# Performance work log

Hardware: AMD Instinct MI355X
Metric: run time of the kernel (lower is better)

The kernel has to match this reference:

```python
import jax, jax.numpy as jnp
import numpy as np

D = 384; NH = 4; FF = 1024; NL = 2
L_ENC = 750; T_AUD = 1500; VOCAB = 60; T_TXT = 256; B = 8; S_SPK = 8; GAMA = 1.0


def _conv1d(x, w, b, stride):
    y = jax.lax.conv_general_dilated(x, w, (stride,), [(1, 1)], dimension_numbers=("NCH", "OIH", "NCH"))
    return y + b[None, :, None]


def _ln(x, g, b):
    m = x.mean(-1, keepdims=True)
    v = ((x - m) ** 2).mean(-1, keepdims=True)
    return (x - m) * jax.lax.rsqrt(v + 1e-5) * g + b


def _enc_layer(x, qkv_w, qkv_b, ow, ob, f1w, f1b, f2w, f2b, g1, b1, g2, b2):
    Bq, L, d = x.shape
    hd = d // NH
    q, k, v = jnp.split(x @ qkv_w.T + qkv_b, 3, axis=-1)
    q = q.reshape(Bq, L, NH, hd); k = k.reshape(Bq, L, NH, hd); v = v.reshape(Bq, L, NH, hd)
    s = jnp.einsum("blhd,bmhd->bhlm", q, k) * np.float32(1.0 / np.sqrt(hd))
    a = jax.nn.softmax(s, axis=-1)
    ctx = jnp.einsum("bhlm,bmhd->blhd", a, v).reshape(Bq, L, d)
    x = _ln(x + ctx @ ow.T + ob, g1, b1)
    h = jax.nn.relu(x @ f1w.T + f1b) @ f2w.T + f2b
    return _ln(x + h, g2, b2)


def _gru(x, h, wih, whh, bih, bhh):
    gi = x @ wih.T + bih
    gh = h @ whh.T + bhh
    ir, iz, inn = jnp.split(gi, 3, axis=-1)
    hr, hz, hn = jnp.split(gh, 3, axis=-1)
    r = jax.nn.sigmoid(ir + hr)
    z = jax.nn.sigmoid(iz + hz)
    n = jnp.tanh(inn + r * hn)
    return (1.0 - z) * n + z * h


def _nll(logits, tgt):
    # torch F.nll_loss applied to raw scores (faithful to source), ignore_index=-100
    valid = (tgt != -100)
    idx = jnp.where(valid, tgt, 0)
    picked = jnp.take_along_axis(logits, idx[..., None], axis=-1)[..., 0]
    return -(picked * valid).sum() / jnp.maximum(valid.sum(), 1).astype(logits.dtype)


def _forward(fl, target_asr_ids, target_diar_ids, remat=False):
    (input_features, speaker_inventory, conv1_w, conv1_b, conv2_w, conv2_b,
     asr_qkv_w, asr_qkv_b, asr_attn_out_w, asr_attn_out_b, asr_ff1_w, asr_ff1_b,
     asr_ff2_w, asr_ff2_b, asr_ln1_g, asr_ln1_b, asr_ln2_g, asr_ln2_b,
     diar_qkv_w, diar_qkv_b, diar_attn_out_w, diar_attn_out_b, diar_ff1_w, diar_ff1_b,
     diar_ff2_w, diar_ff2_b, diar_ln1_g, diar_ln1_b, diar_ln2_g, diar_ln2_b,
     la_q_w, la_k_w, la_v_w, la_in_b, la_out_w, la_out_b, emb,
     asr_rnn_w_ih, asr_rnn_w_hh, asr_rnn_b_ih, asr_rnn_b_hh,
     diar_rnn_w_ih, diar_rnn_w_hh, diar_rnn_b_ih, diar_rnn_b_hh,
     asr_out_w, asr_out_b, d2a_w, d2a_b, h2a_w, h2a_b) = fl
    x = jax.nn.relu(_conv1d(input_features, conv1_w, conv1_b, 1))
    x = jax.nn.relu(_conv1d(x, conv2_w, conv2_b, 2))
    x = jnp.transpose(x, (0, 2, 1))  # [B, L_ENC, D]
    enc_asr = x
    for l in range(NL):
        enc_asr = _enc_layer(enc_asr, asr_qkv_w[l], asr_qkv_b[l], asr_attn_out_w[l], asr_attn_out_b[l],
                             asr_ff1_w[l], asr_ff1_b[l], asr_ff2_w[l], asr_ff2_b[l],
                             asr_ln1_g[l], asr_ln1_b[l], asr_ln2_g[l], asr_ln2_b[l])
    enc_diar = x
    for l in range(NL):
        enc_diar = _enc_layer(enc_diar, diar_qkv_w[l], diar_qkv_b[l], diar_attn_out_w[l], diar_attn_out_b[l],
                              diar_ff1_w[l], diar_ff1_b[l], diar_ff2_w[l], diar_ff2_b[l],
                              diar_ln1_g[l], diar_ln1_b[l], diar_ln2_g[l], diar_ln2_b[l])
    Bsz = x.shape[0]
    inv_norm = jnp.linalg.norm(speaker_inventory, axis=2)  # [B, S]

    def step(carry, tgt):
        token, asr_ctx, h_asr, h_diar, attns = carry
        e = emb[token]  # [B, D]
        h_asr = _gru(jnp.concatenate([asr_ctx, e], 1), h_asr,
                     asr_rnn_w_ih, asr_rnn_w_hh, asr_rnn_b_ih, asr_rnn_b_hh)
        # 1-dim MultiheadAttention: q=h_asr[:,:,None], k=prev attentions, v=enc_asr (vdim=384->1)
        q = h_asr[:, :, None] * la_q_w[0, 0] + la_in_b[0]   # [B, L, 1]
        k = attns * la_k_w[0, 0] + la_in_b[1]               # [B, L, 1]
        v = enc_asr @ la_v_w.T + la_in_b[2]                 # [B, L, 1]
        s = q @ jnp.swapaxes(k, 1, 2)                       # [B, L, L]; head_dim=1 -> scale 1
        a = jax.nn.softmax(s, axis=-1)
        attns_new = (a @ v) * la_out_w[0, 0] + la_out_b[0]  # [B, L, 1]
        w = attns_new[..., 0]
        asr_ctx_new = jnp.einsum("bld,bl->bd", enc_asr, w)
        spk_ctx = jnp.einsum("bld,bl->bd", enc_diar, w)
        h_diar_new = _gru(jnp.concatenate([spk_ctx, e], 1), h_diar,
                          diar_rnn_w_ih, diar_rnn_w_hh, diar_rnn_b_ih, diar_rnn_b_hh)
        sc = jnp.einsum("bsd,bd->bs", speaker_inventory, h_diar_new)
        hn = jnp.linalg.norm(h_diar_new, axis=1, keepdims=True)
        beta = jax.nn.softmax(sc / (hn * inv_norm), axis=1)
        spk_state = jnp.einsum("bsd,bs->bd", speaker_inventory, beta)
        logits = (asr_ctx_new + h_asr @ h2a_w.T + h2a_b + spk_state @ d2a_w.T + d2a_b) @ asr_out_w.T + asr_out_b
        next_tok = jnp.where(tgt == -100, 0, tgt)
        return (next_tok, asr_ctx_new, h_asr, h_diar_new, attns_new), (logits, beta)

    step_fn = jax.checkpoint(step) if remat else step
    init = (jnp.zeros((Bsz,), jnp.int32),
            jnp.zeros((Bsz, D), jnp.float32),
            jnp.zeros((Bsz, L_ENC), jnp.float32),
            jnp.zeros((Bsz, D), jnp.float32),
            jnp.zeros((Bsz, L_ENC, 1), jnp.float32))
    _, (logits_seq, beta_seq) = jax.lax.scan(step_fn, init, jnp.swapaxes(target_asr_ids, 0, 1))
    asr_outputs = jnp.swapaxes(logits_seq, 0, 1)   # [B, T, VOCAB]
    diar_outputs = jnp.swapaxes(beta_seq, 0, 1)    # [B, T, S]
    loss = _nll(asr_outputs, target_asr_ids) + GAMA * _nll(diar_outputs, target_diar_ids)
    return asr_outputs, diar_outputs, loss


def setup_inputs() -> dict:
    key = jax.random.key(0)
    cnt = [0]
    def p(shape, scale=0.05):
        cnt[0] += 1
        return jax.random.normal(jax.random.fold_in(key, cnt[0]), shape, dtype=jnp.float32) * scale
    inp = {}
    inp["input_features"] = p((B, 80, T_AUD), 1.0)
    inp["speaker_inventory"] = p((B, S_SPK, D), 1.0)
    inp["conv1_w"] = p((D, 80, 3)); inp["conv1_b"] = p((D,))
    inp["conv2_w"] = p((D, D, 3)); inp["conv2_b"] = p((D,))
    for pre in ("asr", "diar"):
        inp[pre + "_qkv_w"] = p((NL, 3 * D, D)); inp[pre + "_qkv_b"] = p((NL, 3 * D))
        inp[pre + "_attn_out_w"] = p((NL, D, D)); inp[pre + "_attn_out_b"] = p((NL, D))
        inp[pre + "_ff1_w"] = p((NL, FF, D)); inp[pre + "_ff1_b"] = p((NL, FF))
        inp[pre + "_ff2_w"] = p((NL, D, FF)); inp[pre + "_ff2_b"] = p((NL, D))
        inp[pre + "_ln1_g"] = jnp.ones((NL, D), jnp.float32); inp[pre + "_ln1_b"] = jnp.zeros((NL, D), jnp.float32)
        inp[pre + "_ln2_g"] = jnp.ones((NL, D), jnp.float32); inp[pre + "_ln2_b"] = jnp.zeros((NL, D), jnp.float32)
    inp["la_q_w"] = p((1, 1), 1.0); inp["la_k_w"] = p((1, 1), 1.0); inp["la_v_w"] = p((1, D))
    inp["la_in_b"] = p((3,)); inp["la_out_w"] = p((1, 1), 1.0); inp["la_out_b"] = p((1,))
    inp["emb"] = p((VOCAB, D), 1.0)
    inp["asr_rnn_w_ih"] = p((3 * L_ENC, 2 * D)); inp["asr_rnn_w_hh"] = p((3 * L_ENC, L_ENC))
    inp["asr_rnn_b_ih"] = p((3 * L_ENC,)); inp["asr_rnn_b_hh"] = p((3 * L_ENC,))
    inp["diar_rnn_w_ih"] = p((3 * D, 2 * D)); inp["diar_rnn_w_hh"] = p((3 * D, D))
    inp["diar_rnn_b_ih"] = p((3 * D,)); inp["diar_rnn_b_hh"] = p((3 * D,))
    inp["asr_out_w"] = p((VOCAB, D)); inp["asr_out_b"] = p((VOCAB,))
    inp["d2a_w"] = p((D, D)); inp["d2a_b"] = p((D,))
    inp["h2a_w"] = p((D, L_ENC)); inp["h2a_b"] = p((D,))
    inp["target_asr_ids"] = jax.random.randint(jax.random.fold_in(key, 9001), (B, T_TXT), 0, VOCAB, dtype=jnp.int32)
    inp["target_diar_ids"] = jax.random.randint(jax.random.fold_in(key, 9002), (B, T_TXT), 0, S_SPK, dtype=jnp.int32)
    return inp


def reference(input_features, speaker_inventory, conv1_w, conv1_b, conv2_w, conv2_b,
              asr_qkv_w, asr_qkv_b, asr_attn_out_w, asr_attn_out_b, asr_ff1_w, asr_ff1_b,
              asr_ff2_w, asr_ff2_b, asr_ln1_g, asr_ln1_b, asr_ln2_g, asr_ln2_b,
              diar_qkv_w, diar_qkv_b, diar_attn_out_w, diar_attn_out_b, diar_ff1_w, diar_ff1_b,
              diar_ff2_w, diar_ff2_b, diar_ln1_g, diar_ln1_b, diar_ln2_g, diar_ln2_b,
              la_q_w, la_k_w, la_v_w, la_in_b, la_out_w, la_out_b, emb,
              asr_rnn_w_ih, asr_rnn_w_hh, asr_rnn_b_ih, asr_rnn_b_hh,
              diar_rnn_w_ih, diar_rnn_w_hh, diar_rnn_b_ih, diar_rnn_b_hh,
              asr_out_w, asr_out_b, d2a_w, d2a_b, h2a_w, h2a_b,
              target_asr_ids, target_diar_ids):
    fl = (input_features, speaker_inventory, conv1_w, conv1_b, conv2_w, conv2_b,
          asr_qkv_w, asr_qkv_b, asr_attn_out_w, asr_attn_out_b, asr_ff1_w, asr_ff1_b,
          asr_ff2_w, asr_ff2_b, asr_ln1_g, asr_ln1_b, asr_ln2_g, asr_ln2_b,
          diar_qkv_w, diar_qkv_b, diar_attn_out_w, diar_attn_out_b, diar_ff1_w, diar_ff1_b,
          diar_ff2_w, diar_ff2_b, diar_ln1_g, diar_ln1_b, diar_ln2_g, diar_ln2_b,
          la_q_w, la_k_w, la_v_w, la_in_b, la_out_w, la_out_b, emb,
          asr_rnn_w_ih, asr_rnn_w_hh, asr_rnn_b_ih, asr_rnn_b_hh,
          diar_rnn_w_ih, diar_rnn_w_hh, diar_rnn_b_ih, diar_rnn_b_hh,
          asr_out_w, asr_out_b, d2a_w, d2a_b, h2a_w, h2a_b)
    return _forward(fl, target_asr_ids, target_diar_ids, remat=False)
```

## Files before the change

### kernel.cpp

```cpp
#include <hip/hip_runtime.h>
#include <math.h>

#define L_ENC 750
#define T_AUD 1500
#define DD    384
#define FF    1024
#define NHH   4
#define HDIM  96
#define VOCAB 60
#define T_TXT 256
#define BB    8
#define NB    480
#define TB    512

static __device__ __forceinline__ float sigmf(float x){ return 1.f/(1.f + __expf(-x)); }

static __device__ __forceinline__ float cld(const float* p){
  return __hip_atomic_load(p, __ATOMIC_RELAXED, __HIP_MEMORY_SCOPE_AGENT);
}
static __device__ __forceinline__ void cst(float* p, float v){
  __hip_atomic_store(p, v, __ATOMIC_RELAXED, __HIP_MEMORY_SCOPE_AGENT);
}

static __device__ __forceinline__ float bf2f(unsigned int v){
  union { unsigned int u; float f; } c; c.u = v << 16; return c.f;
}
static __device__ __forceinline__ unsigned short f2bf(float x){
  union { float f; unsigned int u; } c; c.f = x;
  unsigned int u = c.u + 0x7fffu + ((c.u >> 16) & 1u);
  return (unsigned short)(u >> 16);
}

static constexpr size_t O_X  = 0;
static constexpr size_t O_EA = 2304000;
static constexpr size_t O_ED = 4608000;
static constexpr size_t O_ST = 6912000;
static constexpr size_t oHASR = O_ST + 0;
static constexpr size_t oATT0 = O_ST + 6000;
static constexpr size_t oATT1 = O_ST + 12000;
static constexpr size_t oHD   = O_ST + 18000;
static constexpr size_t oACTX = O_ST + 21072;
static constexpr size_t oSCTX = O_ST + 27216;
static constexpr size_t oPREP = O_ST + 33360;
static constexpr size_t oGIA  = O_ST + 39504;
static constexpr size_t oGHA  = O_ST + 57504;
static constexpr size_t oGID  = O_ST + 75504;
static constexpr size_t oGHD  = O_ST + 84720;
static constexpr size_t oLACC = O_ST + 93936;
static constexpr size_t oVLA  = O_ST + 93944;
static constexpr size_t oINVN = O_ST + 99944;
static constexpr size_t oBAR  = O_ST + 100008;
static constexpr size_t oZ384 = O_ST + 104200;
static constexpr size_t O_SCR = O_ST + 105000;
static constexpr size_t oWIHAT_A = O_SCR + 0;
static constexpr size_t oWHHT_A  = O_SCR + 432000;
static constexpr size_t oWIHAT_D = O_SCR + 1278000;
static constexpr size_t oWHHT_D  = O_SCR + 1499184;
static constexpr size_t oH2ATh   = O_SCR + 1720368;
static constexpr size_t oAOT     = O_SCR + 1864368;
static constexpr size_t oEMBT    = O_SCR + 1887408;
static constexpr size_t oGEA     = O_SCR + 2673840;
static constexpr size_t oGED     = O_SCR + 7281840;
static constexpr size_t oDIB     = O_SCR + 9641136;
static constexpr size_t oEAh     = O_SCR + 9665712;
static constexpr size_t oEDh     = O_SCR + 10817712;
static constexpr size_t oTMPH    = O_SCR + 12000000;

__global__ void transpose_k(const float* __restrict__ in, int ldin, int R, int C,
                            float* __restrict__ out){
  __shared__ float t[32][33];
  int c0 = blockIdx.x*32, r0 = blockIdx.y*32;
  int x = threadIdx.x, y = threadIdx.y;
  for (int i = y; i < 32; i += 8){
    int r = r0 + i, c = c0 + x;
    t[i][x] = (r < R && c < C) ? in[(size_t)r*ldin + c] : 0.f;
  }
  __syncthreads();
  for (int i = y; i < 32; i += 8){
    int c = c0 + i, r = r0 + x;
    if (c < C && r < R) out[(size_t)c*R + r] = t[x][i];
  }
}

__global__ void packTbf_k(const float* __restrict__ in, int ldin, int R, int K,
                          unsigned short* __restrict__ out){
  __shared__ float tl[32][33];
  int k0 = blockIdx.x*32, r0 = blockIdx.y*32;
  int x = threadIdx.x, y = threadIdx.y;
  int K8 = ((K + 7) >> 3) << 3;
  for (int i = y; i < 32; i += 8){
    int r = r0 + i, k = k0 + x;
    tl[i][x] = (r < R && k < K) ? in[(size_t)r*ldin + k] : 0.f;
  }
  __syncthreads();
  for (int i = y; i < 32; i += 8){
    int k = k0 + i, r = r0 + x;
    if (k < K8 && r < R) out[((size_t)(k >> 3)*R + r)*8 + (k & 7)] = f2bf(tl[x][i]);
  }
}

__global__ __launch_bounds__(256) void cvtbf_k(const float* __restrict__ src,
    unsigned short* __restrict__ dst, int n4){
  int i = blockIdx.x*256 + threadIdx.x;
  if (i >= n4) return;
  float4 v = ((const float4*)src)[i];
  ushort4 o; o.x = f2bf(v.x); o.y = f2bf(v.y); o.z = f2bf(v.z); o.w = f2bf(v.w);
  ((ushort4*)dst)[i] = o;
}

__global__ void kt_k(const float* __restrict__ QKV, float* __restrict__ KT){
  __shared__ float t[32][33];
  int z = blockIdx.z; int b = z >> 2, h = z & 3;
  const float* in = QKV + (size_t)b*L_ENC*1152 + 384 + h*HDIM;
  float* out = KT + (size_t)z*HDIM*L_ENC;
  int c0 = blockIdx.x*32, r0 = blockIdx.y*32;
  int x = threadIdx.x, y = threadIdx.y;
  for (int i = y; i < 32; i += 8){
    int r = r0 + i, c = c0 + x;
    t[i][x] = (r < L_ENC && c < HDIM) ? in[(size_t)r*1152 + c] : 0.f;
  }
  __syncthreads();
  for (int i = y; i < 32; i += 8){
    int c = c0 + i, r = r0 + x;
    if (c < HDIM && r < L_ENC) out[(size_t)c*L_ENC + r] = t[x][i];
  }
}

template<int RELU, int HASRES>
__global__ __launch_bounds__(256) void gemm_k(
    const float* __restrict__ A, int lda, const float* __restrict__ W, int ldw,
    const float* __restrict__ bias, const float* __restrict__ Res,
    float* __restrict__ C, int ldc, int M, int N, int K)
{
  __shared__ __align__(16) float As[16][132];
  __shared__ __align__(16) float Ws[16][68];
  int tid = threadIdx.x;
  int row0 = blockIdx.y*128, col0 = blockIdx.x*64;
  int tx = tid & 15, ty = tid >> 4;
  int lr = tid >> 2, lk = (tid & 3)*4;
  float acc[8][4] = {};
  for (int k0 = 0; k0 < K; k0 += 16){
    float4 a0 = make_float4(0,0,0,0), a1 = make_float4(0,0,0,0), w0 = make_float4(0,0,0,0);
    int r0i = row0 + lr, r1i = row0 + 64 + lr, wri = col0 + lr;
    if (r0i < M) a0 = *(const float4*)(A + (size_t)r0i*lda + k0 + lk);
    if (r1i < M) a1 = *(const float4*)(A + (size_t)r1i*lda + k0 + lk);
    if (wri < N) w0 = *(const float4*)(W + (size_t)wri*ldw + k0 + lk);
    As[lk+0][lr] = a0.x; As[lk+1][lr] = a0.y; As[lk+2][lr] = a0.z; As[lk+3][lr] = a0.w;
    As[lk+0][64+lr] = a1.x; As[lk+1][64+lr] = a1.y; As[lk+2][64+lr] = a1.z; As[lk+3][64+lr] = a1.w;
    Ws[lk+0][lr] = w0.x; Ws[lk+1][lr] = w0.y; Ws[lk+2][lr] = w0.z; Ws[lk+3][lr] = w0.w;
    __syncthreads();
    #pragma unroll
    for (int k = 0; k < 16; k++){
      float4 b4 = *(const float4*)&Ws[k][tx*4];
      float4 a4 = *(const float4*)&As[k][ty*8];
      float4 a5 = *(const float4*)&As[k][ty*8+4];
      acc[0][0] += a4.x*b4.x; acc[0][1] += a4.x*b4.y; acc[0][2] += a4.x*b4.z; acc[0][3] += a4.x*b4.w;
      acc[1][0] += a4.y*b4.x; acc[1][1] += a4.y*b4.y; acc[1][2] += a4.y*b4.z; acc[1][3] += a4.y*b4.w;
      acc[2][0] += a4.z*b4.x; acc[2][1] += a4.z*b4.y; acc[2][2] += a4.z*b4.z; acc[2][3] += a4.z*b4.w;
      acc[3][0] += a4.w*b4.x; acc[3][1] += a4.w*b4.y; acc[3][2] += a4.w*b4.z; acc[3][3] += a4.w*b4.w;
      acc[4][0] += a5.x*b4.x; acc[4][1] += a5.x*b4.y; acc[4][2] += a5.x*b4.z; acc[4][3] += a5.x*b4.w;
      acc[5][0] += a5.y*b4.x; acc[5][1] += a5.y*b4.y; acc[5][2] += a5.y*b4.z; acc[5][3] += a5.y*b4.w;
      acc[6][0] += a5.z*b4.x; acc[6][1] += a5.z*b4.y; acc[6][2] += a5.z*b4.z; acc[6][3] += a5.z*b4.w;
      acc[7][0] += a5.w*b4.x; acc[7][1] += a5.w*b4.y; acc[7][2] += a5.w*b4.z; acc[7][3] += a5.w*b4.w;
    }
    __syncthreads();
  }
  #pragma unroll
  for (int ii = 0; ii < 8; ii++){
    int m = row0 + ty*8 + ii;
    if (m >= M) continue;
    #pragma unroll
    for (int jj = 0; jj < 4; jj++){
      int n = col0 + tx*4 + jj;
      if (n >= N) continue;
      float v = acc[ii][jj] + bias[n];
      if (HASRES) v += Res[(size_t)m*ldc + n];
      if (RELU) v = fmaxf(v, 0.f);
      C[(size_t)m*ldc + n] = v;
    }
  }
}

__global__ void im2col1(const float* __restrict__ in, float* __restrict__ P){
  int t = blockIdx.x, b = blockIdx.y, i = threadIdx.x;
  if (i >= 240) return;
  int ic = i/3, kt = i - ic*3;
  int p = t + kt - 1;
  P[((size_t)(b*T_AUD + t))*240 + i] = (p >= 0 && p < T_AUD) ? in[((size_t)(b*80 + ic))*T_AUD + p] : 0.f;
}

__global__ __launch_bounds__(384) void im2col2(const float* __restrict__ X1T, float* __restrict__ P){
  int t = blockIdx.x, b = blockIdx.y, ic = threadIdx.x;
  size_t ob = ((size_t)(b*L_ENC + t))*1152 + (size_t)ic*3;
  #pragma unroll
  for (int kt = 0; kt < 3; kt++){
    int p = 2*t + kt - 1;
    P[ob + kt] = (p >= 0 && p < T_AUD) ? X1T[((size_t)(b*T_AUD + p))*DD + ic] : 0.f;
  }
}

__global__ __launch_bounds__(256) void dup_k(const float* __restrict__ src,
    float* __restrict__ a, float* __restrict__ b){
  size_t i = (size_t)blockIdx.x*256 + threadIdx.x;
  float4 v = ((const float4*)src)[i];
  ((float4*)a)[i] = v;
  ((float4*)b)[i] = v;
}

__global__ __launch_bounds__(128) void ln_k(float* __restrict__ X, const float* __restrict__ g,
                                            const float* __restrict__ bt){
  int r = blockIdx.x, tid = threadIdx.x;
  float* p = X + (size_t)r*DD;
  float v0 = p[tid], v1 = p[tid+128], v2 = p[tid+256];
  __shared__ float red[128];
  red[tid] = v0+v1+v2; __syncthreads();
  for (int k = 64; k > 0; k >>= 1){ if (tid < k) red[tid] += red[tid+k]; __syncthreads(); }
  float m = red[0] * (1.f/384.f);
  __syncthreads();
  float d0 = v0-m, d1 = v1-m, d2 = v2-m;
  red[tid] = d0*d0 + d1*d1 + d2*d2; __syncthreads();
  for (int k = 64; k > 0; k >>= 1){ if (tid < k) red[tid] += red[tid+k]; __syncthreads(); }
  float rs = rsqrtf(red[0]*(1.f/384.f) + 1e-5f);
  p[tid]     = d0*rs*g[tid]     + bt[tid];
  p[tid+128] = d1*rs*g[tid+128] + bt[tid+128];
  p[tid+256] = d2*rs*g[tid+256] + bt[tid+256];
}

__global__ __launch_bounds__(1024) void attn_enc(const float* __restrict__ QKV,
    const float* __restrict__ KT, float* __restrict__ ctx){
  int b = blockIdx.z, h = blockIdx.y, i0 = blockIdx.x*16;
  int tid = threadIdx.x, lane = tid & 63, wv = tid >> 6;
  __shared__ float q_s[16][96];
  __shared__ float p_s[16][752];
  __shared__ float den_s[16];
  for (int idx = tid; idx < 16*96; idx += 1024){
    int r2 = idx/96, c = idx - r2*96; int i = i0 + r2;
    q_s[r2][c] = (i < L_ENC) ? QKV[((size_t)(b*L_ENC + i))*1152 + h*HDIM + c]*0.10206207f : 0.f;
  }
  __syncthreads();
  int i = i0 + wv;
  const float* ktb = KT + ((size_t)(b*4 + h))*HDIM*L_ENC;
  if (i < L_ENC){
    float sr[12] = {0,0,0,0,0,0,0,0,0,0,0,0};
    for (int c = 0; c < 96; c++){
      float qc = q_s[wv][c];
      const float* kr = ktb + c*L_ENC + lane;
      #pragma unroll
      for (int jt = 0; jt < 12; jt++) sr[jt] += qc*kr[jt*64];
    }
    float mx = -1e30f;
    #pragma unroll
    for (int jt = 0; jt < 12; jt++){ if (lane + jt*64 < L_ENC) mx = fmaxf(mx, sr[jt]); }
    #pragma unroll
    for (int o = 32; o > 0; o >>= 1) mx = fmaxf(mx, __shfl_xor(mx, o));
    float den = 0.f;
    #pragma unroll
    for (int jt = 0; jt < 12; jt++){
      int j = lane + jt*64;
      if (j < L_ENC){ float e = __expf(sr[jt]-mx); p_s[wv][j] = e; den += e; }
    }
    #pragma unroll
    for (int o = 32; o > 0; o >>= 1) den += __shfl_xor(den, o);
    if (lane == 0) den_s[wv] = den;
  }
  __syncthreads();
  if (i < L_ENC){
    float idn = 1.f/den_s[wv];
    const float* vb = QKV + (size_t)b*L_ENC*1152 + 768 + h*HDIM;
    float a0 = 0.f, a1 = 0.f;
    for (int j = 0; j < L_ENC; j++){
      float pj = p_s[wv][j];
      const float* vr = vb + (size_t)j*1152;
      a0 += pj*vr[lane];
      if (lane < 32) a1 += pj*vr[lane + 64];
    }
    size_t ob = ((size_t)(b*L_ENC + i))*DD + h*HDIM;
    ctx[ob + lane] = a0*idn;
    if (lane < 32) ctx[ob + lane + 64] = a1*idn;
  }
}

__global__ __launch_bounds__(384) void embed_k(const float* __restrict__ emb,
    const int* __restrict__ tgtA, float* __restrict__ E){
  int row = blockIdx.x; int t = row >> 3, b = row & 7;
  int tok = 0;
  if (t > 0){ int v = tgtA[b*T_TXT + t - 1]; tok = (v == -100) ? 0 : v; }
  E[(size_t)row*DD + threadIdx.x] = emb[(size_t)tok*DD + threadIdx.x];
}

__global__ __launch_bounds__(256) void vla_k(const float* __restrict__ EA,
    const float* __restrict__ lav, const float* __restrict__ lain, float* __restrict__ VLA){
  int row = blockIdx.x*4 + (threadIdx.x >> 6);
  int lane = threadIdx.x & 63;
  if (row >= BB*L_ENC) return;
  const float* p = EA + (size_t)row*DD;
  float s = 0.f;
  for (int d = lane; d < DD; d += 64) s += p[d]*lav[d];
  #pragma unroll
  for (int o = 32; o > 0; o >>= 1) s += __shfl_xor(s, o);
  if (lane == 0) VLA[row] = s + lain[2];
}

__global__ void invn_k(const float* __restrict__ inv, float* __restrict__ INVN){
  int row = blockIdx.x; int lane = threadIdx.x;
  float s = 0.f;
  for (int d = lane; d < DD; d += 64){ float v = inv[(size_t)row*DD + d]; s += v*v; }
  #pragma unroll
  for (int o = 32; o > 0; o >>= 1) s += __shfl_xor(s, o);
  if (lane == 0) INVN[row] = sqrtf(s);
}

struct DecParams {
  float* ws; float* out;
  const float* ABHH; const float* DBHH;
  const float* SPK;  const float* AOB;
  const float* LAQ; const float* LAK; const float* LAIB; const float* LAOW; const float* LAOB;
  const float* H2AB; const float* D2AB;
  const int* TGTA; const int* TGTD;
};

static __device__ __forceinline__ void gbar(unsigned* s, unsigned epoch){
  __syncthreads();
  int tid = threadIdx.x;
  if (blockIdx.x == 0){
    if (tid > 0 && tid < NB){
      while (__hip_atomic_load(&s[tid*4], __ATOMIC_RELAXED, __HIP_MEMORY_SCOPE_AGENT) < epoch)
        __builtin_amdgcn_s_sleep(4);
    }
    __syncthreads();
    if (tid < NB)
      __hip_atomic_store(&s[(512 + tid)*4], epoch, __ATOMIC_RELAXED, __HIP_MEMORY_SCOPE_AGENT);
  } else {
    if (tid == 0){
      __hip_atomic_store(&s[blockIdx.x*4], epoch, __ATOMIC_RELAXED, __HIP_MEMORY_SCOPE_AGENT);
      while (__hip_atomic_load(&s[(512 + blockIdx.x)*4], __ATOMIC_RELAXED, __HIP_MEMORY_SCOPE_AGENT) < epoch)
        __builtin_amdgcn_s_sleep(4);
    }
    __syncthreads();
  }
}

#define FMA8(acc, s_, base) { const float4 b0_ = *(const float4*)&(base)[0]; const float4 b1_ = *(const float4*)&(base)[4]; \
  acc[0]+=b0_.x*(s_); acc[1]+=b0_.y*(s_); acc[2]+=b0_.z*(s_); acc[3]+=b0_.w*(s_); \
  acc[4]+=b1_.x*(s_); acc[5]+=b1_.y*(s_); acc[6]+=b1_.z*(s_); acc[7]+=b1_.w*(s_); }

#define GFMA8(acc, wv_, a_) { \
  FMA8(acc, bf2f(wv_.x & 0xffffu), (a_)+0);  FMA8(acc, bf2f(wv_.x >> 16), (a_)+8); \
  FMA8(acc, bf2f(wv_.y & 0xffffu), (a_)+16); FMA8(acc, bf2f(wv_.y >> 16), (a_)+24); \
  FMA8(acc, bf2f(wv_.z & 0xffffu), (a_)+32); FMA8(acc, bf2f(wv_.z >> 16), (a_)+40); \
  FMA8(acc, bf2f(wv_.w & 0xffffu), (a_)+48); FMA8(acc, bf2f(wv_.w >> 16), (a_)+56); }

#define ACC8(acc, ev_, s_) { \
  acc[0]+=bf2f(ev_.x&0xffffu)*(s_); acc[1]+=bf2f(ev_.x>>16)*(s_); \
  acc[2]+=bf2f(ev_.y&0xffffu)*(s_); acc[3]+=bf2f(ev_.y>>16)*(s_); \
  acc[4]+=bf2f(ev_.z&0xffffu)*(s_); acc[5]+=bf2f(ev_.z>>16)*(s_); \
  acc[6]+=bf2f(ev_.w&0xffffu)*(s_); acc[7]+=bf2f(ev_.w>>16)*(s_); }

template<int NR, int KH, int KOH>
__device__ void gates_fn(int task, const unsigned short* __restrict__ WIT,
                         const unsigned short* __restrict__ WHT,
                         const float* __restrict__ ctxv, const float* __restrict__ hv,
                         const float* __restrict__ GE, const float* __restrict__ bhh,
                         float* __restrict__ GI, float* __restrict__ GH, int t, float* SM)
{
  float* ac  = SM;
  float* hh  = SM + 3072;
  float* pgi = SM + 3072 + KOH*64;
  float* pgh = pgi + 4096;
  int tid = threadIdx.x;
  for (int idx = tid; idx < 3072; idx += TB){ int b = idx/384, k = idx - b*384; ac[k*8+b] = cld(&ctxv[idx]); }
  for (int idx = tid; idx < KH*8;  idx += TB){ int b = idx/KH,  k = idx - b*KH;  hh[k*8+b] = cld(&hv[idx]); }
  for (int idx = KH*8 + tid; idx < KOH*64; idx += TB) hh[idx] = 0.f;
  __syncthreads();
  int rl = tid & 15, kp = tid >> 4;
  int r = task*16 + rl;
  float gi[8] = {}, gh[8] = {};
  if (r < NR){
    const uint4* W4 = (const uint4*)WIT;
    int q0 = (kp*48) >> 5, q1 = ((kp+1)*48) >> 5;
    for (int q = q0; q < q1; q++){
      uint4 wq = W4[(size_t)q*NR + r];
      const float* a = &ac[q*64];
      GFMA8(gi, wq, a);
    }
    const uint4* WH4 = (const uint4*)WHT;
    int h0 = (kp*KOH) >> 5, h1 = ((kp+1)*KOH) >> 5;
    for (int q = h0; q < h1; q++){
      uint4 wq = WH4[(size_t)q*NR + r];
      const float* a = &hh[q*64];
      GFMA8(gh, wq, a);
    }
  }
  #pragma unroll
  for (int b = 0; b < 8; b++){ pgi[(kp*16+rl)*8 + b] = gi[b]; pgh[(kp*16+rl)*8 + b] = gh[b]; }
  __syncthreads();
  if (tid < 128){
    int rl2 = tid & 15, bb = tid >> 4;
    int rr = task*16 + rl2;
    if (rr < NR){
      float s1 = 0.f, s2 = 0.f;
      #pragma unroll
      for (int kq = 0; kq < 32; kq++){ s1 += pgi[(kq*16+rl2)*8+bb]; s2 += pgh[(kq*16+rl2)*8+bb]; }
      cst(&GI[(size_t)bb*NR + rr], s1 + GE[((size_t)t*8 + bb)*NR + rr]);
      cst(&GH[(size_t)bb*NR + rr], s2 + bhh[rr]);
    }
  }
  __syncthreads();
}

__device__ void phase_hattn_ctx(int bid, int t, float* ws,
                                const unsigned short* __restrict__ EAh,
                                const unsigned short* __restrict__ EDh,
                                const unsigned short* __restrict__ H2h,
                                const DecParams& P, float* SM)
{
  float* kk = SM;
  float* vv = SM + 768;
  float* wl = SM + 1536;
  float* hl = SM + 1552;
  float* part = SM + 1568;
  int tid = threadIdx.x;
  int b = bid & 7, chunk = bid >> 3;
  int i0 = chunk*13; int n = L_ENC - i0; if (n > 13) n = 13;
  const float* acur = ws + ((t & 1) ? oATT1 : oATT0);
  float*       anxt = ws + ((t & 1) ? oATT0 : oATT1);
  const float* GIAp = ws + oGIA; const float* GHAp = ws + oGHA;
  float* HASRp = ws + oHASR;
  const float* VLAp = ws + oVLA;
  float kw = P.LAK[0], kb = P.LAIB[1];
  for (int j = tid; j < L_ENC; j += TB){
    kk[j] = cld(&acur[b*L_ENC + j])*kw + kb;
    vv[j] = VLAp[b*L_ENC + j];
  }
  __syncthreads();
  int wv = tid >> 6, lane = tid & 63;
  float laq = P.LAQ[0], li0 = P.LAIB[0], low = P.LAOW[0], lob = P.LAOB[0];
  for (int il = wv; il < n; il += 8){
    int i = i0 + il;
    int base = b*2250 + i;
    float rr = sigmf(cld(&GIAp[base]) + cld(&GHAp[base]));
    float zz = sigmf(cld(&GIAp[base+750]) + cld(&GHAp[base+750]));
    float nn = tanhf(cld(&GIAp[base+1500]) + rr*cld(&GHAp[base+1500]));
    float h = (1.f - zz)*nn + zz*cld(&HASRp[b*L_ENC + i]);
    float q = h*laq + li0;
    float sr[12]; float mx = -1e30f;
    #pragma unroll
    for (int jt = 0; jt < 12; jt++){
      int j = lane + jt*64;
      float s = (j < L_ENC) ? q*kk[j] : -1e30f;
      sr[jt] = s; mx = fmaxf(mx, s);
    }
    #pragma unroll
    for (int o = 32; o > 0; o >>= 1) mx = fmaxf(mx, __shfl_xor(mx, o));
    float se = 0.f, sv = 0.f;
    #pragma unroll
    for (int jt = 0; jt < 12; jt++){
      int j = lane + jt*64;
      if (j < L_ENC){ float e = __expf(sr[jt] - mx); se += e; sv += e*vv[j]; }
    }
    #pragma unroll
    for (int o = 32; o > 0; o >>= 1){ se += __shfl_xor(se, o); sv += __shfl_xor(sv, o); }
    if (lane == 0){
      cst(&HASRp[b*L_ENC + i], h);
      float w = (sv/se)*low + lob;
      cst(&anxt[b*L_ENC + i], w);
      wl[il] = w; hl[il] = h;
    }
  }
  __syncthreads();
  if (tid < 480){
    int lg = tid / 48, oct = tid - lg*48;
    int d0 = oct*8;
    float a8[8] = {}, s8[8] = {}, h8[8] = {};
    for (int j = lg; j < n; j += 10){
      size_t ro = ((size_t)(b*L_ENC + i0 + j))*DD + d0;
      float wj = wl[j], hj = hl[j];
      uint4 e1 = *(const uint4*)&EAh[ro];
      ACC8(a8, e1, wj);
      uint4 e2 = *(const uint4*)&EDh[ro];
      ACC8(s8, e2, wj);
      uint4 e3 = *(const uint4*)&H2h[(size_t)(i0 + j)*DD + d0];
      ACC8(h8, e3, hj);
    }
    float* pp = part + (size_t)(lg*48 + oct)*24;
    #pragma unroll
    for (int e = 0; e < 8; e++){ pp[e] = a8[e]; pp[8+e] = s8[e]; pp[16+e] = h8[e]; }
  }
  __syncthreads();
  if (tid < 96){
    int oct = tid >> 1, e = (tid & 1)*4;
    float ra[4] = {}, rs[4] = {}, rh[4] = {};
    #pragma unroll
    for (int lg = 0; lg < 10; lg++){
      const float* pp = part + (size_t)(lg*48 + oct)*24;
      #pragma unroll
      for (int jj = 0; jj < 4; jj++){
        ra[jj] += pp[e+jj]; rs[jj] += pp[8+e+jj]; rh[jj] += pp[16+e+jj];
      }
    }
    int par = t & 1;
    int d0 = tid*4;
    float* A = &ws[oACTX + par*3072 + b*DD + d0];
    float* S = &ws[oSCTX + par*3072 + b*DD + d0];
    float* Pr = &ws[oPREP + par*3072 + b*DD + d0];
    atomicAdd(&A[0], ra[0]); atomicAdd(&A[1], ra[1]); atomicAdd(&A[2], ra[2]); atomicAdd(&A[3], ra[3]);
    atomicAdd(&S[0], rs[0]); atomicAdd(&S[1], rs[1]); atomicAdd(&S[2], rs[2]); atomicAdd(&S[3], rs[3]);
    atomicAdd(&Pr[0], ra[0]+rh[0]); atomicAdd(&Pr[1], ra[1]+rh[1]);
    atomicAdd(&Pr[2], ra[2]+rh[2]); atomicAdd(&Pr[3], ra[3]+rh[3]);
  }
  __syncthreads();
}

__device__ void phase_final(int b, int t, float* ws, const float* prep,
                            const DecParams& P, float* SM)
{
  float* hd_s = SM;
  float* pre_s = SM + 384;
  float* red = SM + 768;
  float* beta_s = SM + 1280;
  float* sc_s = SM + 1288;
  float* part2 = SM + 1296;
  int tid = threadIdx.x;
  bool act = tid < DD;
  const float* GIDp = ws + oGID; const float* GHDp = ws + oGHD;
  float* HDp = ws + oHD;
  float h = 0.f;
  if (act){
    int base = b*1152 + tid;
    float rr = sigmf(cld(&GIDp[base]) + cld(&GHDp[base]));
    float zz = sigmf(cld(&GIDp[base+384]) + cld(&GHDp[base+384]));
    float nn = tanhf(cld(&GIDp[base+768]) + rr*cld(&GHDp[base+768]));
    h = (1.f - zz)*nn + zz*cld(&HDp[b*DD + tid]);
    hd_s[tid] = h; cst(&HDp[b*DD + tid], h);
  }
  red[tid] = act ? h*h : 0.f;
  __syncthreads();
  for (int s = 256; s > 0; s >>= 1){ if (tid < s) red[tid] += red[tid+s]; __syncthreads(); }
  float hn = sqrtf(red[0]);
  int sg = tid >> 6, lane = tid & 63;
  float ps = 0.f;
  for (int j = lane; j < DD; j += 64) ps += P.SPK[((size_t)(b*8 + sg))*DD + j]*hd_s[j];
  #pragma unroll
  for (int o = 32; o > 0; o >>= 1) ps += __shfl_xor(ps, o);
  if (lane == 0) sc_s[sg] = ps / (hn * ws[oINVN + b*8 + sg]);
  __syncthreads();
  if (tid == 0){
    float mx = -1e30f;
    for (int s2 = 0; s2 < 8; s2++) mx = fmaxf(mx, sc_s[s2]);
    float sm = 0.f;
    for (int s2 = 0; s2 < 8; s2++){ float e = __expf(sc_s[s2] - mx); beta_s[s2] = e; sm += e; }
    float isv = 1.f/sm;
    for (int s2 = 0; s2 < 8; s2++) beta_s[s2] *= isv;
    int td = P.TGTD[b*T_TXT + t];
    if (td != -100){ atomicAdd(&ws[oLACC+2], beta_s[td]); atomicAdd(&ws[oLACC+3], 1.f); }
  }
  __syncthreads();
  if (tid < 8) P.out[122880 + ((size_t)(b*T_TXT + t))*8 + tid] = beta_s[tid];
  if (act){
    float p = cld(&prep[b*DD + tid]);
    const float* Mb = ws + oDIB + (size_t)(b*8)*DD + tid;
    #pragma unroll
    for (int s2 = 0; s2 < 8; s2++) p += beta_s[s2]*Mb[(size_t)s2*DD];
    pre_s[tid] = p;
  }
  __syncthreads();
  {
    int vg = tid >> 6, v = tid & 63;
    float pl = 0.f;
    if (v < VOCAB){
      const float* AOTp = ws + oAOT;
      int d0 = vg*48;
      for (int d2 = d0; d2 < d0+48; d2++) pl += pre_s[d2]*AOTp[d2*VOCAB + v];
    }
    part2[vg*64 + v] = pl;
  }
  __syncthreads();
  if (tid < VOCAB){
    float lg = P.AOB[tid];
    #pragma unroll
    for (int g = 0; g < 8; g++) lg += part2[g*64 + tid];
    P.out[((size_t)(b*T_TXT + t))*VOCAB + tid] = lg;
    int ta = P.TGTA[b*T_TXT + t];
    if (ta == tid) atomicAdd(&ws[oLACC+0], lg);
    if (tid == 0 && ta != -100) atomicAdd(&ws[oLACC+1], 1.f);
  }
  __syncthreads();
}

__global__ __launch_bounds__(TB, 4) void dec_loop(DecParams P)
{
  __shared__ __align__(16) float SM[17280];
  int bid = blockIdx.x;
  float* ws = P.ws;
  unsigned* slots = (unsigned*)(ws + oBAR);
  unsigned ep = 0;
  const unsigned short* WIA = (const unsigned short*)(ws + oWIHAT_A);
  const unsigned short* WHA = (const unsigned short*)(ws + oWHHT_A);
  const unsigned short* WID = (const unsigned short*)(ws + oWIHAT_D);
  const unsigned short* WHD = (const unsigned short*)(ws + oWHHT_D);
  const unsigned short* EAh = (const unsigned short*)(ws + oEAh);
  const unsigned short* EDh = (const unsigned short*)(ws + oEDh);
  const unsigned short* H2h = (const unsigned short*)(ws + oH2ATh);

  if (bid < 141)
    gates_fn<2250,750,94>(bid, WIA, WHA, ws+oACTX, ws+oHASR,
                          ws+oGEA, P.ABHH, ws+oGIA, ws+oGHA, 0, SM);
  else if (bid < 149){
    int b = bid - 141;
    for (int d = threadIdx.x; d < DD; d += TB)
      cst(&ws[oPREP + b*DD + d], P.H2AB[d] + P.D2AB[d]);
  }
  gbar(slots, ++ep);

  for (int t = 0; t <= T_TXT; t++){
    if (t < T_TXT && bid < 464) phase_hattn_ctx(bid, t, ws, EAh, EDh, H2h, P, SM);
    else if (bid >= 464 && bid < 472 && t >= 1)
      phase_final(bid - 464, t - 1, ws, ws + oPREP + ((t-1) & 1)*3072, P, SM);
    gbar(slots, ++ep);
    if (t == T_TXT) break;

    if (bid < 72)
      gates_fn<1152,384,48>(bid, WID, WHD, ws+oSCTX+(t&1)*3072, ws+oHD,
                            ws+oGED, P.DBHH, ws+oGID, ws+oGHD, t, SM);
    else if (bid < 213){
      if (t + 1 < T_TXT)
        gates_fn<2250,750,94>(bid-72, WIA, WHA, ws+oACTX+(t&1)*3072, ws+oHASR,
                              ws+oGEA, P.ABHH, ws+oGIA, ws+oGHA, t+1, SM);
    } else if (bid < 221 && t + 1 < T_TXT){
      int b = bid - 213, par = (t + 1) & 1;
      for (int d = threadIdx.x; d < DD; d += TB){
        cst(&ws[oACTX + par*3072 + b*DD + d], 0.f);
        cst(&ws[oSCTX + par*3072 + b*DD + d], 0.f);
        cst(&ws[oPREP + par*3072 + b*DD + d], P.H2AB[d] + P.D2AB[d]);
      }
    }
    gbar(slots, ++ep);
  }
}

__global__ void loss_final_k(const float* __restrict__ lacc, float* __restrict__ out){
  if (threadIdx.x == 0 && blockIdx.x == 0){
    float la = lacc[0]/fmaxf(lacc[1], 1.f);
    float ld = lacc[2]/fmaxf(lacc[3], 1.f);
    out[139264] = -(la + ld);
  }
}

extern "C" void kernel_launch(void* const* d_in, const int* in_sizes, int n_in,
                              void* d_out, int out_size, void* d_ws, size_t ws_size,
                              hipStream_t stream)
{
  (void)in_sizes; (void)n_in; (void)out_size; (void)ws_size;
  float* ws  = (float*)d_ws;
  float* out = (float*)d_out;

  const float* IN0   = (const float*)d_in[0];
  const float* SPK   = (const float*)d_in[1];
  const float* C1W   = (const float*)d_in[2];
  const float* C1B   = (const float*)d_in[3];
  const float* C2W   = (const float*)d_in[4];
  const float* C2B   = (const float*)d_in[5];
  const float* LAQ   = (const float*)d_in[30];
  const float* LAK   = (const float*)d_in[31];
  const float* LAV   = (const float*)d_in[32];
  const float* LAIB  = (const float*)d_in[33];
  const float* LAOW  = (const float*)d_in[34];
  const float* LAOB  = (const float*)d_in[35];
  const float* EMB   = (const float*)d_in[36];
  const float* AWIH  = (const float*)d_in[37];
  const float* AWHH  = (const float*)d_in[38];
  const float* ABIH  = (const float*)d_in[39];
  const float* ABHH  = (const float*)d_in[40];
  const float* DWIH  = (const float*)d_in[41];
  const float* DWHH  = (const float*)d_in[42];
  const float* DBIH  = (const float*)d_in[43];
  const float* DBHH  = (const float*)d_in[44];
  const float* AOW   = (const float*)d_in[45];
  const float* AOB   = (const float*)d_in[46];
  const float* D2AW  = (const float*)d_in[47];
  const float* D2AB  = (const float*)d_in[48];
  const float* H2AW  = (const float*)d_in[49];
  const float* H2AB  = (const float*)d_in[50];
  const int*   TGTA  = (const int*)d_in[51];
  const int*   TGTD  = (const int*)d_in[52];

  const size_t S_QKV = O_SCR;
  const size_t S_KT  = O_SCR + 6912000;
  const size_t S_CTX = O_SCR + 9216000;
  const size_t S_Y   = O_SCR + 11520000;
  const size_t S_H   = O_SCR + 13824000;
  const size_t X1T   = S_KT;
  const size_t Pc1   = S_H;
  const size_t Pc2   = S_QKV;

  hipMemsetAsync((void*)(ws + O_ST), 0, 105000*sizeof(float), stream);

  im2col1<<<dim3(1500,8), 256, 0, stream>>>(IN0, ws + Pc1);
  gemm_k<1,0><<<dim3(6,94), 256, 0, stream>>>(ws+Pc1, 240, C1W, 240, C1B, nullptr, ws+X1T, 384, 12000, 384, 240);
  im2col2<<<dim3(750,8), 384, 0, stream>>>(ws+X1T, ws+Pc2);
  gemm_k<1,0><<<dim3(6,47), 256, 0, stream>>>(ws+Pc2, 1152, C2W, 1152, C2B, nullptr, ws+O_X, 384, 6000, 384, 1152);

  dup_k<<<2250, 256, 0, stream>>>(ws+O_X, ws+O_EA, ws+O_ED);

  auto enc_layer = [&](float* Xb, const float* qw, const float* qb, const float* ow,
                       const float* ob, const float* f1w, const float* f1b,
                       const float* f2w, const float* f2b,
                       const float* g1, const float* b1, const float* g2, const float* b2){
    gemm_k<0,0><<<dim3(18,47), 256, 0, stream>>>(Xb, 384, qw, 384, qb, nullptr, ws+S_QKV, 1152, 6000, 1152, 384);
    kt_k<<<dim3(3,24,32), dim3(32,8), 0, stream>>>(ws+S_QKV, ws+S_KT);
    attn_enc<<<dim3(47,4,8), 1024, 0, stream>>>(ws+S_QKV, ws+S_KT, ws+S_CTX);
    gemm_k<0,1><<<dim3(6,47), 256, 0, stream>>>(ws+S_CTX, 384, ow, 384, ob, Xb, ws+S_Y, 384, 6000, 384, 384);
    ln_k<<<6000, 128, 0, stream>>>(ws+S_Y, g1, b1);
    gemm_k<1,0><<<dim3(16,47), 256, 0, stream>>>(ws+S_Y, 384, f1w, 384, f1b, nullptr, ws+S_H, 1024, 6000, 1024, 384);
    gemm_k<0,1><<<dim3(6,47), 256, 0, stream>>>(ws+S_H, 1024, f2w, 1024, f2b, ws+S_Y, Xb, 384, 6000, 384, 1024);
    ln_k<<<6000, 128, 0, stream>>>(Xb, g2, b2);
  };
  for (int st = 0; st < 2; st++){
    int base = (st == 0) ? 6 : 18;
    float* Xb = ws + ((st == 0) ? O_EA : O_ED);
    const float* qkvw = (const float*)d_in[base+0];
    const float* qkvb = (const float*)d_in[base+1];
    const float* aow  = (const float*)d_in[base+2];
    const float* aob2 = (const float*)d_in[base+3];
    const float* f1w  = (const float*)d_in[base+4];
    const float* f1b  = (const float*)d_in[base+5];
    const float* f2w  = (const float*)d_in[base+6];
    const float* f2b  = (const float*)d_in[base+7];
    const float* g1   = (const float*)d_in[base+8];
    const float* b1   = (const float*)d_in[base+9];
    const float* g2   = (const float*)d_in[base+10];
    const float* b2   = (const float*)d_in[base+11];
    for (int l = 0; l < 2; l++){
      enc_layer(Xb, qkvw + (size_t)l*1152*384, qkvb + (size_t)l*1152,
                aow + (size_t)l*384*384, aob2 + (size_t)l*384,
                f1w + (size_t)l*1024*384, f1b + (size_t)l*1024,
                f2w + (size_t)l*384*1024, f2b + (size_t)l*384,
                g1 + (size_t)l*384, b1 + (size_t)l*384, g2 + (size_t)l*384, b2 + (size_t)l*384);
    }
  }

  packTbf_k<<<dim3(12,71), dim3(32,8), 0, stream>>>(AWIH, 768, 2250, 384, (unsigned short*)(ws+oWIHAT_A));
  packTbf_k<<<dim3(24,71), dim3(32,8), 0, stream>>>(AWHH, 750, 2250, 750, (unsigned short*)(ws+oWHHT_A));
  packTbf_k<<<dim3(12,36), dim3(32,8), 0, stream>>>(DWIH, 768, 1152, 384, (unsigned short*)(ws+oWIHAT_D));
  packTbf_k<<<dim3(12,36), dim3(32,8), 0, stream>>>(DWHH, 384, 1152, 384, (unsigned short*)(ws+oWHHT_D));
  transpose_k<<<dim3(24,12), dim3(32,8), 0, stream>>>(H2AW, 750, 384, 750, ws+oTMPH);
  cvtbf_k<<<282, 256, 0, stream>>>(ws+oTMPH, (unsigned short*)(ws+oH2ATh), 72000);
  transpose_k<<<dim3(12,2),  dim3(32,8), 0, stream>>>(AOW, 384, 60, 384, ws+oAOT);
  embed_k<<<2048, 384, 0, stream>>>(EMB, TGTA, ws+oEMBT);
  gemm_k<0,0><<<dim3(36,16), 256, 0, stream>>>(ws+oEMBT, 384, AWIH+384, 768, ABIH, nullptr, ws+oGEA, 2250, 2048, 2250, 384);
  gemm_k<0,0><<<dim3(18,16), 256, 0, stream>>>(ws+oEMBT, 384, DWIH+384, 768, DBIH, nullptr, ws+oGED, 1152, 2048, 1152, 384);
  gemm_k<0,0><<<dim3(6,1), 256, 0, stream>>>(SPK, 384, D2AW, 384, ws+oZ384, nullptr, ws+oDIB, 384, 64, 384, 384);
  vla_k<<<1500, 256, 0, stream>>>(ws+O_EA, LAV, LAIB, ws+oVLA);
  invn_k<<<64, 64, 0, stream>>>(SPK, ws+oINVN);
  cvtbf_k<<<2250, 256, 0, stream>>>(ws+O_EA, (unsigned short*)(ws+oEAh), 576000);
  cvtbf_k<<<2250, 256, 0, stream>>>(ws+O_ED, (unsigned short*)(ws+oEDh), 576000);

  DecParams DP;
  DP.ws = ws; DP.out = out;
  DP.ABHH = ABHH; DP.DBHH = DBHH; DP.SPK = SPK; DP.AOB = AOB;
  DP.LAQ = LAQ; DP.LAK = LAK; DP.LAIB = LAIB; DP.LAOW = LAOW; DP.LAOB = LAOB;
  DP.H2AB = H2AB; DP.D2AB = D2AB; DP.TGTA = TGTA; DP.TGTD = TGTD;
  dec_loop<<<dim3(NB), dim3(TB), 0, stream>>>(DP);

  loss_final_k<<<1, 64, 0, stream>>>(ws+oLACC, out);
}
```

Baseline: 21.25 ms.

## Split attention and context reduction into separate phases without atomics

```diff
diff --git a/kernel.cpp b/kernel.cpp
--- a/kernel.cpp
+++ b/kernel.cpp
@@ -350,12 +350,6 @@
   FMA8(acc, bf2f(wv_.z & 0xffffu), (a_)+32); FMA8(acc, bf2f(wv_.z >> 16), (a_)+40); \
   FMA8(acc, bf2f(wv_.w & 0xffffu), (a_)+48); FMA8(acc, bf2f(wv_.w >> 16), (a_)+56); }
 
-#define ACC8(acc, ev_, s_) { \
-  acc[0]+=bf2f(ev_.x&0xffffu)*(s_); acc[1]+=bf2f(ev_.x>>16)*(s_); \
-  acc[2]+=bf2f(ev_.y&0xffffu)*(s_); acc[3]+=bf2f(ev_.y>>16)*(s_); \
-  acc[4]+=bf2f(ev_.z&0xffffu)*(s_); acc[5]+=bf2f(ev_.z>>16)*(s_); \
-  acc[6]+=bf2f(ev_.w&0xffffu)*(s_); acc[7]+=bf2f(ev_.w>>16)*(s_); }
-
 template<int NR, int KH, int KOH>
 __device__ void gates_fn(int task, const unsigned short* __restrict__ WIT,
                          const unsigned short* __restrict__ WHT,
@@ -408,17 +402,10 @@
   __syncthreads();
 }
 
-__device__ void phase_hattn_ctx(int bid, int t, float* ws,
-                                const unsigned short* __restrict__ EAh,
-                                const unsigned short* __restrict__ EDh,
-                                const unsigned short* __restrict__ H2h,
-                                const DecParams& P, float* SM)
+__device__ void phase_hattn(int bid, int t, float* ws, const DecParams& P, float* SM)
 {
   float* kk = SM;
   float* vv = SM + 768;
-  float* wl = SM + 1536;
-  float* hl = SM + 1552;
-  float* part = SM + 1568;
   int tid = threadIdx.x;
   int b = bid & 7, chunk = bid >> 3;
   int i0 = chunk*13; int n = L_ENC - i0; if (n > 13) n = 13;
@@ -462,51 +449,58 @@
     for (int o = 32; o > 0; o >>= 1){ se += __shfl_xor(se, o); sv += __shfl_xor(sv, o); }
     if (lane == 0){
       cst(&HASRp[b*L_ENC + i], h);
-      float w = (sv/se)*low + lob;
-      cst(&anxt[b*L_ENC + i], w);
-      wl[il] = w; hl[il] = h;
-    }
-  }
-  __syncthreads();
-  if (tid < 480){
-    int lg = tid / 48, oct = tid - lg*48;
-    int d0 = oct*8;
-    float a8[8] = {}, s8[8] = {}, h8[8] = {};
-    for (int j = lg; j < n; j += 10){
-      size_t ro = ((size_t)(b*L_ENC + i0 + j))*DD + d0;
-      float wj = wl[j], hj = hl[j];
-      uint4 e1 = *(const uint4*)&EAh[ro];
-      ACC8(a8, e1, wj);
-      uint4 e2 = *(const uint4*)&EDh[ro];
-      ACC8(s8, e2, wj);
-      uint4 e3 = *(const uint4*)&H2h[(size_t)(i0 + j)*DD + d0];
-      ACC8(h8, e3, hj);
-    }
-    float* pp = part + (size_t)(lg*48 + oct)*24;
-    #pragma unroll
-    for (int e = 0; e < 8; e++){ pp[e] = a8[e]; pp[8+e] = s8[e]; pp[16+e] = h8[e]; }
-  }
-  __syncthreads();
-  if (tid < 96){
-    int oct = tid >> 1, e = (tid & 1)*4;
-    float ra[4] = {}, rs[4] = {}, rh[4] = {};
-    #pragma unroll
-    for (int lg = 0; lg < 10; lg++){
-      const float* pp = part + (size_t)(lg*48 + oct)*24;
-      #pragma unroll
-      for (int jj = 0; jj < 4; jj++){
-        ra[jj] += pp[e+jj]; rs[jj] += pp[8+e+jj]; rh[jj] += pp[16+e+jj];
-      }
-    }
-    int par = t & 1;
-    int d0 = tid*4;
-    float* A = &ws[oACTX + par*3072 + b*DD + d0];
-    float* S = &ws[oSCTX + par*3072 + b*DD + d0];
-    float* Pr = &ws[oPREP + par*3072 + b*DD + d0];
-    atomicAdd(&A[0], ra[0]); atomicAdd(&A[1], ra[1]); atomicAdd(&A[2], ra[2]); atomicAdd(&A[3], ra[3]);
-    atomicAdd(&S[0], rs[0]); atomicAdd(&S[1], rs[1]); atomicAdd(&S[2], rs[2]); atomicAdd(&S[3], rs[3]);
-    atomicAdd(&Pr[0], ra[0]+rh[0]); atomicAdd(&Pr[1], ra[1]+rh[1]);
-    atomicAdd(&Pr[2], ra[2]+rh[2]); atomicAdd(&Pr[3], ra[3]+rh[3]);
+      cst(&anxt[b*L_ENC + i], (sv/se)*low + lob);
+    }
+  }
+  __syncthreads();
+}
+
+__device__ void phase_ctx(int bid, int t, float* ws,
+                          const unsigned short* __restrict__ EAh,
+                          const unsigned short* __restrict__ EDh,
+                          const unsigned short* __restrict__ H2h,
+                          const DecParams& P, float* SM)
+{
+  float* wl   = SM;
+  float* hl   = SM + 768;
+  float* reda = SM + 1536;
+  float* reds = SM + 2048;
+  float* redh = SM + 2560;
+  int tid = threadIdx.x;
+  int b = bid & 7, dc = bid >> 3;
+  int d0 = dc*32;
+  const float* anxt = ws + ((t & 1) ? oATT0 : oATT1);
+  const float* HASRp = ws + oHASR;
+  for (int j = tid; j < L_ENC; j += TB){
+    wl[j] = cld(&anxt[b*L_ENC + j]);
+    hl[j] = cld(&HASRp[b*L_ENC + j]);
+  }
+  __syncthreads();
+  int ls = tid >> 5, dx = tid & 31;
+  int d = d0 + dx;
+  const unsigned short* EAb = EAh + (size_t)b*L_ENC*DD + d;
+  const unsigned short* EDb = EDh + (size_t)b*L_ENC*DD + d;
+  const unsigned short* H2b = H2h + d;
+  float a = 0.f, s = 0.f, hp = 0.f;
+  for (int l = ls; l < L_ENC; l += 16){
+    size_t lo = (size_t)l*DD;
+    float wj = wl[l], hj = hl[l];
+    a  += bf2f(EAb[lo])*wj;
+    s  += bf2f(EDb[lo])*wj;
+    hp += bf2f(H2b[lo])*hj;
+  }
+  reda[tid] = a; reds[tid] = s; redh[tid] = hp;
+  __syncthreads();
+  if (tid < 32){
+    float ra = 0.f, rs = 0.f, rh = 0.f;
+    #pragma unroll
+    for (int q = 0; q < 16; q++){
+      ra += reda[q*32+tid]; rs += reds[q*32+tid]; rh += redh[q*32+tid];
+    }
+    int dd = d0 + tid;
+    cst(&ws[oACTX + b*DD + dd], ra);
+    cst(&ws[oSCTX + b*DD + dd], rs);
+    cst(&ws[oPREP + b*DD + dd], P.H2AB[dd] + P.D2AB[dd] + ra + rh);
   }
   __syncthreads();
 }
@@ -605,35 +599,24 @@
   if (bid < 141)
     gates_fn<2250,750,94>(bid, WIA, WHA, ws+oACTX, ws+oHASR,
                           ws+oGEA, P.ABHH, ws+oGIA, ws+oGHA, 0, SM);
-  else if (bid < 149){
-    int b = bid - 141;
-    for (int d = threadIdx.x; d < DD; d += TB)
-      cst(&ws[oPREP + b*DD + d], P.H2AB[d] + P.D2AB[d]);
-  }
   gbar(slots, ++ep);
 
   for (int t = 0; t <= T_TXT; t++){
-    if (t < T_TXT && bid < 464) phase_hattn_ctx(bid, t, ws, EAh, EDh, H2h, P, SM);
+    if (t < T_TXT && bid < 464) phase_hattn(bid, t, ws, P, SM);
     else if (bid >= 464 && bid < 472 && t >= 1)
-      phase_final(bid - 464, t - 1, ws, ws + oPREP + ((t-1) & 1)*3072, P, SM);
+      phase_final(bid - 464, t - 1, ws, ws + oPREP, P, SM);
     gbar(slots, ++ep);
     if (t == T_TXT) break;
 
+    if (bid < 96) phase_ctx(bid, t, ws, EAh, EDh, H2h, P, SM);
+    gbar(slots, ++ep);
+
     if (bid < 72)
-      gates_fn<1152,384,48>(bid, WID, WHD, ws+oSCTX+(t&1)*3072, ws+oHD,
+      gates_fn<1152,384,48>(bid, WID, WHD, ws+oSCTX, ws+oHD,
                             ws+oGED, P.DBHH, ws+oGID, ws+oGHD, t, SM);
-    else if (bid < 213){
-      if (t + 1 < T_TXT)
-        gates_fn<2250,750,94>(bid-72, WIA, WHA, ws+oACTX+(t&1)*3072, ws+oHASR,
-                              ws+oGEA, P.ABHH, ws+oGIA, ws+oGHA, t+1, SM);
-    } else if (bid < 221 && t + 1 < T_TXT){
-      int b = bid - 213, par = (t + 1) & 1;
-      for (int d = threadIdx.x; d < DD; d += TB){
-        cst(&ws[oACTX + par*3072 + b*DD + d], 0.f);
-        cst(&ws[oSCTX + par*3072 + b*DD + d], 0.f);
-        cst(&ws[oPREP + par*3072 + b*DD + d], P.H2AB[d] + P.D2AB[d]);
-      }
-    }
+    else if (bid < 213 && t + 1 < T_TXT)
+      gates_fn<2250,750,94>(bid-72, WIA, WHA, ws+oACTX, ws+oHASR,
+                            ws+oGEA, P.ABHH, ws+oGIA, ws+oGHA, t+1, SM);
     gbar(slots, ++ep);
   }
 }
```

Measured after the change: 23.08 ms. +8.6%, slower.
